# Optimization experiments

Hardware: AMD Instinct MI355X
Metric: run time of the kernel (lower is better)

## Reference

```python
import jax, jax.numpy as jnp
import numpy as np

ALPHA = 0.2
NEG_BIG = -9e15

def setup_inputs() -> dict:
    key = jax.random.key(0)
    k1, k2, k3, k4 = jax.random.split(key, 4)
    B, N, F = 8, 2048, 256
    h = jax.random.normal(k1, (B, N, F), dtype=jnp.float32)
    adj = jax.random.randint(k2, (B, N, N), 0, 2, dtype=jnp.int32)
    W = jax.random.normal(k3, (F, F), dtype=jnp.float32) * (1.414 / jnp.sqrt(F))
    a = jax.random.normal(k4, (2 * F, 1), dtype=jnp.float32) * 0.1
    return {"h": h, "adj": adj, "W": W, "a": a}

def reference(h, adj, W, a):
    F_out = W.shape[1]
    Wh = jnp.einsum('bnf,fo->bno', h, W)            # [B,N,F]
    Wh1 = Wh @ a[:F_out]                             # [B,N,1]
    Wh2 = Wh @ a[F_out:]                             # [B,N,1]
    e = jax.nn.leaky_relu(Wh1 + jnp.swapaxes(Wh2, 1, 2), negative_slope=ALPHA)  # [B,N,N]
    scores = jnp.where(adj > 0, e, NEG_BIG)
    attention = jax.nn.softmax(scores, axis=-1)      # [B,N,N]
    h_prime = jnp.einsum('bnm,bmf->bnf', attention, Wh)
    out = h + jax.nn.elu(h_prime)                    # concat=True -> elu; residual add
    return (out, attention)
```

## Files before the change

### kernel.cpp

```cpp
#include <hip/hip_runtime.h>

#define NB 8
#define NN 2048
#define NF 256

typedef __attribute__((ext_vector_type(8))) short bf16x8;
typedef __attribute__((ext_vector_type(4))) float f32x4;

__device__ __forceinline__ unsigned short f2bf(float x) {
  union { float f; unsigned int i; } c; c.f = x;
  unsigned int r = c.i + 0x7FFFu + ((c.i >> 16) & 1u);
  return (unsigned short)(r >> 16);
}
__device__ __forceinline__ unsigned short f2bf_fast(float x) {
  union { float f; unsigned int i; } c; c.f = x;
  return (unsigned short)((c.i + 0x8000u) >> 16);
}
__device__ __forceinline__ bf16x8 cvt8(float4 c0, float4 c1) {
  union { bf16x8 v8; unsigned short us[8]; } cu;
  cu.us[0] = f2bf_fast(c0.x); cu.us[1] = f2bf_fast(c0.y);
  cu.us[2] = f2bf_fast(c0.z); cu.us[3] = f2bf_fast(c0.w);
  cu.us[4] = f2bf_fast(c1.x); cu.us[5] = f2bf_fast(c1.y);
  cu.us[6] = f2bf_fast(c1.z); cu.us[7] = f2bf_fast(c1.w);
  return cu.v8;
}

__global__ __launch_bounds__(256) void k_prep(
    const float* __restrict__ W, const float* __restrict__ a,
    unsigned short* __restrict__ WT, float* __restrict__ u, float* __restrict__ v) {
  int t = threadIdx.x;
  if (blockIdx.x < 256) {
    int k = blockIdx.x;
    WT[t * 256 + k] = f2bf(W[k * 256 + t]);
  } else {
    float su = 0.f, sv = 0.f;
    for (int o = 0; o < 256; ++o) {
      float w = W[t * 256 + o];
      su += w * a[o];
      sv += w * a[256 + o];
    }
    u[t] = su; v[t] = sv;
  }
}

__global__ __launch_bounds__(256) void k_wht(
    const float* __restrict__ h, const unsigned short* __restrict__ WTr,
    unsigned short* __restrict__ WhT) {
  int bx = blockIdx.x;
  int b = bx >> 5;
  int t = bx & 31;
  int fBlk = (t >> 3) * 64;
  int iBlk = (t & 7) * 256;
  int wave = threadIdx.x >> 6, lane = threadIdx.x & 63;
  int fW = fBlk + (wave >> 1) * 32;
  int iW = iBlk + (wave & 1) * 128;
  int l15 = lane & 15, q8 = (lane >> 4) * 8;
  const float* hB = h + (size_t)b * NN * NF;

  f32x4 acc[2][8];
#pragma unroll
  for (int mt = 0; mt < 2; ++mt)
#pragma unroll
    for (int nt = 0; nt < 8; ++nt)
      acc[mt][nt] = (f32x4){0.f, 0.f, 0.f, 0.f};

  for (int k0 = 0; k0 < NF; k0 += 32) {
    int kk = k0 + q8;
    bf16x8 af[2], bfr[8];
#pragma unroll
    for (int mt = 0; mt < 2; ++mt) {
      int f = fW + mt * 16 + l15;
      af[mt] = *(const bf16x8*)(WTr + f * 256 + kk);
    }
#pragma unroll
    for (int nt = 0; nt < 8; ++nt) {
      int i = iW + nt * 16 + l15;
      const float* p = hB + (size_t)i * NF + kk;
      bfr[nt] = cvt8(*(const float4*)p, *(const float4*)(p + 4));
    }
#pragma unroll
    for (int mt = 0; mt < 2; ++mt)
#pragma unroll
      for (int nt = 0; nt < 8; ++nt)
        acc[mt][nt] = __builtin_amdgcn_mfma_f32_16x16x32_bf16(af[mt], bfr[nt], acc[mt][nt], 0, 0, 0);
  }

  unsigned short* WhTb = WhT + (size_t)b * NF * NN;
  int q4 = (lane >> 4) * 4;
#pragma unroll
  for (int mt = 0; mt < 2; ++mt)
#pragma unroll
    for (int nt = 0; nt < 8; ++nt)
#pragma unroll
      for (int r = 0; r < 4; ++r) {
        int f = fW + mt * 16 + q4 + r;
        int i = iW + nt * 16 + l15;
        WhTb[(size_t)f * NN + i] = f2bf(acc[mt][nt][r]);
      }
}

__global__ __launch_bounds__(256) void k_proj(
    const float* __restrict__ h, const float* __restrict__ u,
    const float* __restrict__ v, float* __restrict__ Wh1, float* __restrict__ Wh2) {
  int row = blockIdx.x * 4 + (threadIdx.x >> 6);
  int lane = threadIdx.x & 63;
  float4 hv = *(const float4*)(h + (size_t)row * NF + lane * 4);
  const float* up = u + lane * 4;
  const float* vp = v + lane * 4;
  float su = hv.x * up[0] + hv.y * up[1] + hv.z * up[2] + hv.w * up[3];
  float sv = hv.x * vp[0] + hv.y * vp[1] + hv.z * vp[2] + hv.w * vp[3];
#pragma unroll
  for (int off = 32; off >= 1; off >>= 1) {
    su += __shfl_xor(su, off);
    sv += __shfl_xor(sv, off);
  }
  if (lane == 0) { Wh1[row] = su; Wh2[row] = sv; }
}

__global__ __launch_bounds__(256) void k_attn(
    const int* __restrict__ adj, const float* __restrict__ Wh1,
    const float* __restrict__ Wh2, float* __restrict__ att) {
  const float NEGBIG = -9.0e15f;
  int row = blockIdx.x;
  int b = row >> 11;
  int tid = threadIdx.x;
  int lane = tid & 63, wave = tid >> 6;
  const int* arow = adj + (size_t)row * NN;
  const float* w2 = Wh2 + ((size_t)b << 11);
  float w1 = Wh1[row];
  int j0 = tid * 8;

  int4 a0 = *(const int4*)(arow + j0);
  int4 a1 = *(const int4*)(arow + j0 + 4);
  float4 p0 = *(const float4*)(w2 + j0);
  float4 p1 = *(const float4*)(w2 + j0 + 4);

  float s[8];
  {
    float x;
    x = w1 + p0.x; x = x >= 0.f ? x : 0.2f * x; s[0] = (a0.x > 0) ? x : NEGBIG;
    x = w1 + p0.y; x = x >= 0.f ? x : 0.2f * x; s[1] = (a0.y > 0) ? x : NEGBIG;
    x = w1 + p0.z; x = x >= 0.f ? x : 0.2f * x; s[2] = (a0.z > 0) ? x : NEGBIG;
    x = w1 + p0.w; x = x >= 0.f ? x : 0.2f * x; s[3] = (a0.w > 0) ? x : NEGBIG;
    x = w1 + p1.x; x = x >= 0.f ? x : 0.2f * x; s[4] = (a1.x > 0) ? x : NEGBIG;
    x = w1 + p1.y; x = x >= 0.f ? x : 0.2f * x; s[5] = (a1.y > 0) ? x : NEGBIG;
    x = w1 + p1.z; x = x >= 0.f ? x : 0.2f * x; s[6] = (a1.z > 0) ? x : NEGBIG;
    x = w1 + p1.w; x = x >= 0.f ? x : 0.2f * x; s[7] = (a1.w > 0) ? x : NEGBIG;
  }

  float m = s[0];
#pragma unroll
  for (int k = 1; k < 8; ++k) m = fmaxf(m, s[k]);
#pragma unroll
  for (int off = 32; off >= 1; off >>= 1) m = fmaxf(m, __shfl_xor(m, off));

  __shared__ float redA[4], redB[4];
  if (lane == 0) redA[wave] = m;
  __syncthreads();
  m = fmaxf(fmaxf(redA[0], redA[1]), fmaxf(redA[2], redA[3]));

  float e[8];
  float sum = 0.f;
#pragma unroll
  for (int k = 0; k < 8; ++k) { e[k] = __expf(s[k] - m); sum += e[k]; }
#pragma unroll
  for (int off = 32; off >= 1; off >>= 1) sum += __shfl_xor(sum, off);
  if (lane == 0) redB[wave] = sum;
  __syncthreads();
  sum = (redB[0] + redB[1]) + (redB[2] + redB[3]);
  float inv = 1.0f / sum;

  float4 o0 = make_float4(e[0] * inv, e[1] * inv, e[2] * inv, e[3] * inv);
  float4 o1 = make_float4(e[4] * inv, e[5] * inv, e[6] * inv, e[7] * inv);
  float* orow = att + (size_t)row * NN + j0;
  *(float4*)(orow) = o0;
  *(float4*)(orow + 4) = o1;
}

__global__ __launch_bounds__(256) void k_out(
    const float* __restrict__ att, const unsigned short* __restrict__ WhT,
    const float* __restrict__ h, float* __restrict__ out) {
  int bx = blockIdx.x;
  int b = bx >> 5;
  int iBlk = (bx & 31) * 64;
  int wave = threadIdx.x >> 6, lane = threadIdx.x & 63;
  int iW = iBlk + (wave >> 1) * 32;
  int fW = (wave & 1) * 128;
  int l15 = lane & 15, q8 = (lane >> 4) * 8;
  const float* attB = att + (size_t)b * NN * NN;
  const unsigned short* WTb = WhT + (size_t)b * NF * NN;

  f32x4 acc[2][8];
#pragma unroll
  for (int mt = 0; mt < 2; ++mt)
#pragma unroll
    for (int nt = 0; nt < 8; ++nt)
      acc[mt][nt] = (f32x4){0.f, 0.f, 0.f, 0.f};

  for (int j0 = 0; j0 < NN; j0 += 32) {
    int kk = j0 + q8;
    bf16x8 af[2], bfr[8];
#pragma unroll
    for (int mt = 0; mt < 2; ++mt) {
      int i = iW + mt * 16 + l15;
      const float* p = attB + (size_t)i * NN + kk;
      af[mt] = cvt8(*(const float4*)p, *(const float4*)(p + 4));
    }
#pragma unroll
    for (int nt = 0; nt < 8; ++nt) {
      int f = fW + nt * 16 + l15;
      bfr[nt] = *(const bf16x8*)(WTb + (size_t)f * NN + kk);
    }
#pragma unroll
    for (int mt = 0; mt < 2; ++mt)
#pragma unroll
      for (int nt = 0; nt < 8; ++nt)
        acc[mt][nt] = __builtin_amdgcn_mfma_f32_16x16x32_bf16(af[mt], bfr[nt], acc[mt][nt], 0, 0, 0);
  }

  int q4 = (lane >> 4) * 4;
#pragma unroll
  for (int mt = 0; mt < 2; ++mt)
#pragma unroll
    for (int nt = 0; nt < 8; ++nt)
#pragma unroll
      for (int r = 0; r < 4; ++r) {
        int i = iW + mt * 16 + q4 + r;
        int f = fW + nt * 16 + l15;
        size_t idx = ((size_t)(b * NN + i)) * NF + f;
        float hp = acc[mt][nt][r];
        float el = hp > 0.f ? hp : expm1f(hp);
        out[idx] = h[idx] + el;
      }
}

extern "C" void kernel_launch(void* const* d_in, const int* in_sizes, int n_in,
                              void* d_out, int out_size, void* d_ws, size_t ws_size,
                              hipStream_t stream) {
  const float* h = nullptr; const int* adj = nullptr;
  const float* W = nullptr; const float* a = nullptr;
  for (int i = 0; i < n_in; ++i) {
    int s = in_sizes[i];
    if (s == NB * NN * NF) h = (const float*)d_in[i];
    else if (s == NB * NN * NN) adj = (const int*)d_in[i];
    else if (s == NF * NF) W = (const float*)d_in[i];
    else if (s == 2 * NF) a = (const float*)d_in[i];
  }

  float* out = (float*)d_out;
  float* att = out + (size_t)NB * NN * NF;

  char* ws = (char*)d_ws;
  unsigned short* WhT = (unsigned short*)ws;
  unsigned short* WTr = (unsigned short*)(ws + 8388608);
  float* u   = (float*)(ws + 8388608 + 131072);
  float* v   = u + 256;
  float* Wh1 = v + 256;
  float* Wh2 = Wh1 + NB * NN;

  k_prep<<<257, 256, 0, stream>>>(W, a, WTr, u, v);
  k_wht<<<256, 256, 0, stream>>>(h, WTr, WhT);
  k_proj<<<NB * NN / 4, 256, 0, stream>>>(h, u, v, Wh1, Wh2);
  k_attn<<<NB * NN, 256, 0, stream>>>(adj, Wh1, Wh2, att);
  k_out<<<256, 256, 0, stream>>>(att, WhT, h, out);
}
```

Baseline: 428.2 us.

## Use one wave per softmax row and halve GEMM tiles to double block count

The attention softmax kernel now gives each 64-lane wave a whole row (32 values per lane), so reductions stay inside the wave and the shared-memory reductions and block barriers go away. Both MFMA GEMM kernels (Wh projection and attention-times-Wh) shrink the per-wave tile from 32x128 to 32x64 and launch 512 blocks instead of 256, to give the 256-CU part more blocks in flight. The price is more redundant operand loads per output in the GEMMs, with less reuse of the converted attention/h fragments, and more registers per lane in the softmax.

Result: faster. 419.7 us (-2.0%).

```diff
diff --git a/kernel.cpp b/kernel.cpp
--- a/kernel.cpp
+++ b/kernel.cpp
@@ -47,33 +47,33 @@
     const float* __restrict__ h, const unsigned short* __restrict__ WTr,
     unsigned short* __restrict__ WhT) {
   int bx = blockIdx.x;
-  int b = bx >> 5;
-  int t = bx & 31;
-  int fBlk = (t >> 3) * 64;
-  int iBlk = (t & 7) * 256;
+  int b = bx >> 6;
+  int t = bx & 63;
+  int fBlk = (t >> 4) * 64;
+  int iBlk = (t & 15) * 128;
   int wave = threadIdx.x >> 6, lane = threadIdx.x & 63;
   int fW = fBlk + (wave >> 1) * 32;
-  int iW = iBlk + (wave & 1) * 128;
+  int iW = iBlk + (wave & 1) * 64;
   int l15 = lane & 15, q8 = (lane >> 4) * 8;
   const float* hB = h + (size_t)b * NN * NF;
 
-  f32x4 acc[2][8];
-#pragma unroll
-  for (int mt = 0; mt < 2; ++mt)
-#pragma unroll
-    for (int nt = 0; nt < 8; ++nt)
+  f32x4 acc[2][4];
+#pragma unroll
+  for (int mt = 0; mt < 2; ++mt)
+#pragma unroll
+    for (int nt = 0; nt < 4; ++nt)
       acc[mt][nt] = (f32x4){0.f, 0.f, 0.f, 0.f};
 
   for (int k0 = 0; k0 < NF; k0 += 32) {
     int kk = k0 + q8;
-    bf16x8 af[2], bfr[8];
+    bf16x8 af[2], bfr[4];
 #pragma unroll
     for (int mt = 0; mt < 2; ++mt) {
       int f = fW + mt * 16 + l15;
       af[mt] = *(const bf16x8*)(WTr + f * 256 + kk);
     }
 #pragma unroll
-    for (int nt = 0; nt < 8; ++nt) {
+    for (int nt = 0; nt < 4; ++nt) {
       int i = iW + nt * 16 + l15;
       const float* p = hB + (size_t)i * NF + kk;
       bfr[nt] = cvt8(*(const float4*)p, *(const float4*)(p + 4));
@@ -81,7 +81,7 @@
 #pragma unroll
     for (int mt = 0; mt < 2; ++mt)
 #pragma unroll
-      for (int nt = 0; nt < 8; ++nt)
+      for (int nt = 0; nt < 4; ++nt)
         acc[mt][nt] = __builtin_amdgcn_mfma_f32_16x16x32_bf16(af[mt], bfr[nt], acc[mt][nt], 0, 0, 0);
   }
 
@@ -90,7 +90,7 @@
 #pragma unroll
   for (int mt = 0; mt < 2; ++mt)
 #pragma unroll
-    for (int nt = 0; nt < 8; ++nt)
+    for (int nt = 0; nt < 4; ++nt)
 #pragma unroll
       for (int r = 0; r < 4; ++r) {
         int f = fW + mt * 16 + q4 + r;
@@ -121,85 +121,71 @@
     const int* __restrict__ adj, const float* __restrict__ Wh1,
     const float* __restrict__ Wh2, float* __restrict__ att) {
   const float NEGBIG = -9.0e15f;
-  int row = blockIdx.x;
+  int wave = threadIdx.x >> 6, lane = threadIdx.x & 63;
+  int row = blockIdx.x * 4 + wave;
   int b = row >> 11;
-  int tid = threadIdx.x;
-  int lane = tid & 63, wave = tid >> 6;
   const int* arow = adj + (size_t)row * NN;
   const float* w2 = Wh2 + ((size_t)b << 11);
   float w1 = Wh1[row];
-  int j0 = tid * 8;
-
-  int4 a0 = *(const int4*)(arow + j0);
-  int4 a1 = *(const int4*)(arow + j0 + 4);
-  float4 p0 = *(const float4*)(w2 + j0);
-  float4 p1 = *(const float4*)(w2 + j0 + 4);
-
-  float s[8];
-  {
+
+  float s[32];
+#pragma unroll
+  for (int c = 0; c < 8; ++c) {
+    int j = c * 256 + lane * 4;
+    int4 av = *(const int4*)(arow + j);
+    float4 pv = *(const float4*)(w2 + j);
     float x;
-    x = w1 + p0.x; x = x >= 0.f ? x : 0.2f * x; s[0] = (a0.x > 0) ? x : NEGBIG;
-    x = w1 + p0.y; x = x >= 0.f ? x : 0.2f * x; s[1] = (a0.y > 0) ? x : NEGBIG;
-    x = w1 + p0.z; x = x >= 0.f ? x : 0.2f * x; s[2] = (a0.z > 0) ? x : NEGBIG;
-    x = w1 + p0.w; x = x >= 0.f ? x : 0.2f * x; s[3] = (a0.w > 0) ? x : NEGBIG;
-    x = w1 + p1.x; x = x >= 0.f ? x : 0.2f * x; s[4] = (a1.x > 0) ? x : NEGBIG;
-    x = w1 + p1.y; x = x >= 0.f ? x : 0.2f * x; s[5] = (a1.y > 0) ? x : NEGBIG;
-    x = w1 + p1.z; x = x >= 0.f ? x : 0.2f * x; s[6] = (a1.z > 0) ? x : NEGBIG;
-    x = w1 + p1.w; x = x >= 0.f ? x : 0.2f * x; s[7] = (a1.w > 0) ? x : NEGBIG;
+    x = w1 + pv.x; x = x >= 0.f ? x : 0.2f * x; s[c * 4 + 0] = (av.x > 0) ? x : NEGBIG;
+    x = w1 + pv.y; x = x >= 0.f ? x : 0.2f * x; s[c * 4 + 1] = (av.y > 0) ? x : NEGBIG;
+    x = w1 + pv.z; x = x >= 0.f ? x : 0.2f * x; s[c * 4 + 2] = (av.z > 0) ? x : NEGBIG;
+    x = w1 + pv.w; x = x >= 0.f ? x : 0.2f * x; s[c * 4 + 3] = (av.w > 0) ? x : NEGBIG;
   }
 
   float m = s[0];
 #pragma unroll
-  for (int k = 1; k < 8; ++k) m = fmaxf(m, s[k]);
+  for (int k = 1; k < 32; ++k) m = fmaxf(m, s[k]);
 #pragma unroll
   for (int off = 32; off >= 1; off >>= 1) m = fmaxf(m, __shfl_xor(m, off));
 
-  __shared__ float redA[4], redB[4];
-  if (lane == 0) redA[wave] = m;
-  __syncthreads();
-  m = fmaxf(fmaxf(redA[0], redA[1]), fmaxf(redA[2], redA[3]));
-
-  float e[8];
   float sum = 0.f;
 #pragma unroll
-  for (int k = 0; k < 8; ++k) { e[k] = __expf(s[k] - m); sum += e[k]; }
+  for (int k = 0; k < 32; ++k) { s[k] = __expf(s[k] - m); sum += s[k]; }
 #pragma unroll
   for (int off = 32; off >= 1; off >>= 1) sum += __shfl_xor(sum, off);
-  if (lane == 0) redB[wave] = sum;
-  __syncthreads();
-  sum = (redB[0] + redB[1]) + (redB[2] + redB[3]);
   float inv = 1.0f / sum;
 
-  float4 o0 = make_float4(e[0] * inv, e[1] * inv, e[2] * inv, e[3] * inv);
-  float4 o1 = make_float4(e[4] * inv, e[5] * inv, e[6] * inv, e[7] * inv);
-  float* orow = att + (size_t)row * NN + j0;
-  *(float4*)(orow) = o0;
-  *(float4*)(orow + 4) = o1;
+  float* orow = att + (size_t)row * NN;
+#pragma unroll
+  for (int c = 0; c < 8; ++c) {
+    int j = c * 256 + lane * 4;
+    float4 o = make_float4(s[c * 4 + 0] * inv, s[c * 4 + 1] * inv,
+                           s[c * 4 + 2] * inv, s[c * 4 + 3] * inv);
+    *(float4*)(orow + j) = o;
+  }
 }
 
 __global__ __launch_bounds__(256) void k_out(
     const float* __restrict__ att, const unsigned short* __restrict__ WhT,
     const float* __restrict__ h, float* __restrict__ out) {
   int bx = blockIdx.x;
-  int b = bx >> 5;
-  int iBlk = (bx & 31) * 64;
+  int b = bx >> 6;
+  int iW = (bx & 63) * 32;
   int wave = threadIdx.x >> 6, lane = threadIdx.x & 63;
-  int iW = iBlk + (wave >> 1) * 32;
-  int fW = (wave & 1) * 128;
+  int fW = wave * 64;
   int l15 = lane & 15, q8 = (lane >> 4) * 8;
   const float* attB = att + (size_t)b * NN * NN;
   const unsigned short* WTb = WhT + (size_t)b * NF * NN;
 
-  f32x4 acc[2][8];
-#pragma unroll
-  for (int mt = 0; mt < 2; ++mt)
-#pragma unroll
-    for (int nt = 0; nt < 8; ++nt)
+  f32x4 acc[2][4];
+#pragma unroll
+  for (int mt = 0; mt < 2; ++mt)
+#pragma unroll
+    for (int nt = 0; nt < 4; ++nt)
       acc[mt][nt] = (f32x4){0.f, 0.f, 0.f, 0.f};
 
   for (int j0 = 0; j0 < NN; j0 += 32) {
     int kk = j0 + q8;
-    bf16x8 af[2], bfr[8];
+    bf16x8 af[2], bfr[4];
 #pragma unroll
     for (int mt = 0; mt < 2; ++mt) {
       int i = iW + mt * 16 + l15;
@@ -207,14 +193,14 @@
       af[mt] = cvt8(*(const float4*)p, *(const float4*)(p + 4));
     }
 #pragma unroll
-    for (int nt = 0; nt < 8; ++nt) {
+    for (int nt = 0; nt < 4; ++nt) {
       int f = fW + nt * 16 + l15;
       bfr[nt] = *(const bf16x8*)(WTb + (size_t)f * NN + kk);
     }
 #pragma unroll
     for (int mt = 0; mt < 2; ++mt)
 #pragma unroll
-      for (int nt = 0; nt < 8; ++nt)
+      for (int nt = 0; nt < 4; ++nt)
         acc[mt][nt] = __builtin_amdgcn_mfma_f32_16x16x32_bf16(af[mt], bfr[nt], acc[mt][nt], 0, 0, 0);
   }
 
@@ -222,7 +208,7 @@
 #pragma unroll
   for (int mt = 0; mt < 2; ++mt)
 #pragma unroll
-    for (int nt = 0; nt < 8; ++nt)
+    for (int nt = 0; nt < 4; ++nt)
 #pragma unroll
       for (int r = 0; r < 4; ++r) {
         int i = iW + mt * 16 + q4 + r;
@@ -259,8 +245,8 @@
   float* Wh2 = Wh1 + NB * NN;
 
   k_prep<<<257, 256, 0, stream>>>(W, a, WTr, u, v);
-  k_wht<<<256, 256, 0, stream>>>(h, WTr, WhT);
+  k_wht<<<512, 256, 0, stream>>>(h, WTr, WhT);
   k_proj<<<NB * NN / 4, 256, 0, stream>>>(h, u, v, Wh1, Wh2);
-  k_attn<<<NB * NN, 256, 0, stream>>>(adj, Wh1, Wh2, att);
-  k_out<<<256, 256, 0, stream>>>(att, WhT, h, out);
-}
+  k_attn<<<NB * NN / 4, 256, 0, stream>>>(adj, Wh1, Wh2, att);
+  k_out<<<512, 256, 0, stream>>>(att, WhT, h, out);
+}
```
